# Kernel optimization log

Measured on AMD Instinct MI355X. Metric: run time of the kernel, lower is better.

Reference implementation:

```python
import jax, jax.numpy as jnp
import numpy as np

B, T, D = 32, 1024, 512
H = 1024          # hidden_size
LV = 128          # level_hidden_size
NREP = H // LV    # n_repeat = 8
NL = 2            # num_layers


def setup_inputs() -> dict:
    key = jax.random.key(0)
    ks = jax.random.split(key, 9)
    s = 0.02
    inp = {"x": jax.random.normal(ks[0], (B, T, D), jnp.float32)}
    # layer 0: input dim D; layer 1: input dim H
    inp["W_lstm0"] = jax.random.normal(ks[1], (4 * H, D + H), jnp.float32) * s
    inp["b_lstm0"] = jnp.zeros((4 * H,), jnp.float32)
    inp["W_lvl0"] = jax.random.normal(ks[2], (2 * LV, D + H), jnp.float32) * s
    inp["b_lvl0"] = jnp.zeros((2 * LV,), jnp.float32)
    inp["W_lstm1"] = jax.random.normal(ks[3], (4 * H, H + H), jnp.float32) * s
    inp["b_lstm1"] = jnp.zeros((4 * H,), jnp.float32)
    inp["W_lvl1"] = jax.random.normal(ks[4], (2 * LV, H + H), jnp.float32) * s
    inp["b_lvl1"] = jnp.zeros((2 * LV,), jnp.float32)
    return inp


def _cell(Wl, bl, Wv, bv, h, c, x_t):
    comb = jnp.concatenate([x_t, h], axis=-1)               # [B, in+H]
    gates = comb @ Wl.T + bl                                 # [B, 4H]
    cc_i, cc_f, cc_o, cc_g = jnp.split(gates, 4, axis=-1)
    lvl = comb @ Wv.T + bv                                   # [B, 2*LV]
    cc_i_h, cc_f_h = jnp.split(lvl, 2, axis=-1)
    i = jax.nn.sigmoid(cc_i)
    f = jax.nn.sigmoid(cc_f)
    o = jax.nn.sigmoid(cc_o)
    g = jnp.tanh(cc_g)
    p_f = jax.nn.softmax(cc_f_h, axis=-1)
    p_i = jax.nn.softmax(cc_i_h[..., ::-1], axis=-1)
    i_h = jnp.cumsum(p_f, axis=-1)                           # master input gate
    f_h = jnp.cumsum(p_i, axis=-1)[..., ::-1]                # master forget gate
    i_h = jnp.repeat(i_h, NREP, axis=-1)                     # [B, H]
    f_h = jnp.repeat(f_h, NREP, axis=-1)
    w = i_h * f_h
    c_new = w * (f * c + i * g) + (f_h - w) * c + (i_h - w) * g
    h_new = o * jnp.tanh(c_new)
    return h_new, c_new


def _run_layer(Wl, bl, Wv, bv, x):
    # x: [B, T, in]
    bsz = x.shape[0]
    h0 = jnp.zeros((bsz, H), x.dtype)
    c0 = jnp.zeros((bsz, H), x.dtype)

    def step(carry, x_t):
        h, c = carry
        h, c = _cell(Wl, bl, Wv, bv, h, c, x_t)
        return (h, c), h

    (_, _), hs = jax.lax.scan(step, (h0, c0), jnp.swapaxes(x, 0, 1))
    return jnp.swapaxes(hs, 0, 1)                            # [B, T, H]


def reference(x, W_lstm0, b_lstm0, W_lvl0, b_lvl0,
              W_lstm1, b_lstm1, W_lvl1, b_lvl1):
    out0 = _run_layer(W_lstm0, b_lstm0, W_lvl0, b_lvl0, x)
    out1 = _run_layer(W_lstm1, b_lstm1, W_lvl1, b_lvl1, out0)
    return out1
```

## Files before the change

kernel.cpp:

```cpp
#include <hip/hip_runtime.h>

namespace {
constexpr int kB  = 32;
constexpr int kT  = 1024;
constexpr int kD  = 512;
constexpr int kH  = 1024;
constexpr int kLV = 128;
constexpr int kNG = 4 * kH + 2 * kLV;
constexpr int kNBLK = 256;
constexpr int kNTHR = 512;
constexpr int kOffH0 = 8192;
constexpr int kOffWF = kOffH0 + 2 * kB * kH + 2 * kB * kNG;
constexpr int kRedOff = 3 * 1536 * 2 * 16;
constexpr int kIhOff  = kRedOff + 12288;
constexpr int kFhOff  = kIhOff + 512;
constexpr int kSmxOff = kFhOff + 512;
constexpr int kLdsBytes = kSmxOff + 32;
}

typedef float vfloat4 __attribute__((ext_vector_type(4)));
typedef float floatx4 __attribute__((ext_vector_type(4)));
typedef _Float16 half8_t __attribute__((ext_vector_type(8)));
typedef unsigned short ushort_t;

static __device__ __forceinline__ unsigned ld_flag(const unsigned* p) {
  return __hip_atomic_load(p, __ATOMIC_RELAXED, __HIP_MEMORY_SCOPE_AGENT);
}
static __device__ __forceinline__ void st_flag(unsigned* p, unsigned v) {
  __hip_atomic_store(p, v, __ATOMIC_RELAXED, __HIP_MEMORY_SCOPE_AGENT);
}
static __device__ __forceinline__ float ld_coh(const float* p) {
  return __hip_atomic_load(p, __ATOMIC_RELAXED, __HIP_MEMORY_SCOPE_AGENT);
}
static __device__ __forceinline__ void st_wt(float* p, float v) {
  asm volatile("global_store_dword %0, %1, off sc0 sc1" :: "v"(p), "v"(v) : "memory");
}
static __device__ __forceinline__ void st_wtu(unsigned* p, unsigned v) {
  asm volatile("global_store_dword %0, %1, off sc0 sc1" :: "v"(p), "v"(v) : "memory");
}
static __device__ __forceinline__ void ld8h(uint4 v[8], const ushort_t* b) {
  asm volatile(
      "global_load_dwordx4 %0, %8, off sc0 sc1\n\t"
      "global_load_dwordx4 %1, %8, off offset:256 sc0 sc1\n\t"
      "global_load_dwordx4 %2, %8, off offset:512 sc0 sc1\n\t"
      "global_load_dwordx4 %3, %8, off offset:768 sc0 sc1\n\t"
      "global_load_dwordx4 %4, %8, off offset:1024 sc0 sc1\n\t"
      "global_load_dwordx4 %5, %8, off offset:1280 sc0 sc1\n\t"
      "global_load_dwordx4 %6, %8, off offset:1536 sc0 sc1\n\t"
      "global_load_dwordx4 %7, %8, off offset:1792 sc0 sc1\n\t"
      "s_waitcnt vmcnt(0)"
      : "=&v"(v[0]), "=&v"(v[1]), "=&v"(v[2]), "=&v"(v[3]),
        "=&v"(v[4]), "=&v"(v[5]), "=&v"(v[6]), "=&v"(v[7])
      : "v"(b)
      : "memory");
}
static __device__ __forceinline__ void ld8h2(uint4 v[8], uint4 w[8],
                                             const ushort_t* b0, const ushort_t* b1) {
  asm volatile(
      "global_load_dwordx4 %0,  %16, off sc0 sc1\n\t"
      "global_load_dwordx4 %1,  %16, off offset:256 sc0 sc1\n\t"
      "global_load_dwordx4 %2,  %16, off offset:512 sc0 sc1\n\t"
      "global_load_dwordx4 %3,  %16, off offset:768 sc0 sc1\n\t"
      "global_load_dwordx4 %4,  %16, off offset:1024 sc0 sc1\n\t"
      "global_load_dwordx4 %5,  %16, off offset:1280 sc0 sc1\n\t"
      "global_load_dwordx4 %6,  %16, off offset:1536 sc0 sc1\n\t"
      "global_load_dwordx4 %7,  %16, off offset:1792 sc0 sc1\n\t"
      "global_load_dwordx4 %8,  %17, off sc0 sc1\n\t"
      "global_load_dwordx4 %9,  %17, off offset:256 sc0 sc1\n\t"
      "global_load_dwordx4 %10, %17, off offset:512 sc0 sc1\n\t"
      "global_load_dwordx4 %11, %17, off offset:768 sc0 sc1\n\t"
      "global_load_dwordx4 %12, %17, off offset:1024 sc0 sc1\n\t"
      "global_load_dwordx4 %13, %17, off offset:1280 sc0 sc1\n\t"
      "global_load_dwordx4 %14, %17, off offset:1536 sc0 sc1\n\t"
      "global_load_dwordx4 %15, %17, off offset:1792 sc0 sc1\n\t"
      "s_waitcnt vmcnt(0)"
      : "=&v"(v[0]), "=&v"(v[1]), "=&v"(v[2]), "=&v"(v[3]),
        "=&v"(v[4]), "=&v"(v[5]), "=&v"(v[6]), "=&v"(v[7]),
        "=&v"(w[0]), "=&v"(w[1]), "=&v"(w[2]), "=&v"(w[3]),
        "=&v"(w[4]), "=&v"(w[5]), "=&v"(w[6]), "=&v"(w[7])
      : "v"(b0), "v"(b1)
      : "memory");
}
static __device__ __forceinline__ unsigned pkrtz(float a, float b) {
  return __builtin_bit_cast(unsigned, __builtin_amdgcn_cvt_pkrtz(a, b));
}
static __device__ __forceinline__ uint4 pack2(vfloat4 a, vfloat4 b) {
  uint4 r;
  r.x = pkrtz(a.x, a.y); r.y = pkrtz(a.z, a.w);
  r.z = pkrtz(b.x, b.y); r.w = pkrtz(b.z, b.w);
  return r;
}
static __device__ __forceinline__ floatx4 mfma16(uint4 a, uint4 b, floatx4 c) {
  return __builtin_amdgcn_mfma_f32_16x16x32_f16(
      __builtin_bit_cast(half8_t, a), __builtin_bit_cast(half8_t, b), c, 0, 0, 0);
}

__global__ __launch_bounds__(256) void cvt_fp16_kernel(
    const float* __restrict__ src, ushort_t* __restrict__ dst, int n8) {
  int i = blockIdx.x * 256 + threadIdx.x;
  if (i >= n8) return;
  const vfloat4* s4 = (const vfloat4*)src;
  vfloat4 a = s4[2 * i], b = s4[2 * i + 1];
  typedef _Float16 h8 __attribute__((ext_vector_type(8)));
  h8 o;
  o[0] = (_Float16)a.x; o[1] = (_Float16)a.y;
  o[2] = (_Float16)a.z; o[3] = (_Float16)a.w;
  o[4] = (_Float16)b.x; o[5] = (_Float16)b.y;
  o[6] = (_Float16)b.z; o[7] = (_Float16)b.w;
  ((h8*)dst)[i] = o;
}

__global__ __launch_bounds__(kNTHR, 2) void onlstm_kernel(
    const float* __restrict__ x,
    const float* __restrict__ bl0, const float* __restrict__ bv0,
    const float* __restrict__ bl1, const float* __restrict__ bv1,
    const ushort_t* __restrict__ wf0u, const ushort_t* __restrict__ wf1u,
    float* __restrict__ out, float* __restrict__ ws)
{
  const int tid = threadIdx.x;
  const int bid = blockIdx.x;

  unsigned* flagA = (unsigned*)ws;
  unsigned* flagB = (unsigned*)ws + 4096;
  ushort_t* h0f = (ushort_t*)(ws + kOffH0);
  ushort_t* h1f = h0f + kB * kH;
  float* gates0 = ws + kOffH0 + kB * kH;
  float* gates1 = gates0 + kB * kNG;

  __shared__ __align__(16) char sb[kLdsBytes];
  uint4* wb4   = (uint4*)sb;
  float* redp  = (float*)(sb + kRedOff);
  float* ih_sh = (float*)(sb + kIhOff);
  float* fh_sh = (float*)(sb + kFhOff);
  float* smx   = (float*)(sb + kSmxOff);

  auto signal = [&](unsigned* arr, unsigned v) {
    asm volatile("s_waitcnt vmcnt(0)" ::: "memory");
    __syncthreads();
    if (tid == 0) st_flag(&arr[bid * 16], v);
  };
  auto wait_set = [&](unsigned* arr, int lo, int n, unsigned target) {
    if (tid < n) {
      while (ld_flag(&arr[(lo + tid) * 16]) != target)
        __builtin_amdgcn_s_sleep(2);
    }
    __syncthreads();
    asm volatile("" ::: "memory");
  };

  int L, ntile, cb0;
  if (bid < 32)       { L = 0; ntile = 3; cb0 = bid * 48; }
  else if (bid < 120) { L = 0; ntile = 2; cb0 = 1536 + (bid - 32) * 32; }
  else                { L = 1; ntile = 2; cb0 = (bid - 120) * 32; }
  const int K   = L ? 2048 : 1536;
  const int ts4 = K * 2;
  const bool three = (ntile == 3);
  const int rstride = three ? 3 : 2;
  const ushort_t* wf = L ? wf1u : wf0u;
  const float* blp = L ? bl1 : bl0;
  const float* bvp = L ? bv1 : bv0;
  float* gatesL = L ? gates1 : gates0;

  const int lane = tid & 63;
  const int rt   = (tid >> 6) & 1;
  const int str  = tid >> 7;
  const int r_   = rt * 16 + (lane & 15);
  const int koct = lane >> 4;
  const int colg0 = cb0 + (lane & 15);
  const int colg1 = cb0 + 16 + (lane & 15);
  const int colg2 = cb0 + 32 + (lane & 15);

  auto redsl = [&](int slot, int accIdx) -> float* {
    return &redp[(((slot * 2 + rt) * rstride) + accIdx) * 256 + lane * 4];
  };

  for (int tt = 0; tt < ntile; ++tt) {
    const int colb = cb0 + tt * 16;
    for (int idx = tid; idx < ts4; idx += kNTHR) {
      int m = idx >> 6, l2 = idx & 63;
      size_t off = (size_t)(colb + (l2 & 15)) * K + m * 32 + 8 * (l2 >> 4);
      wb4[tt * ts4 + idx] = *(const uint4*)(wf + off);
    }
  }
  const float b0w = (colg0 < 4096) ? blp[colg0] : bvp[colg0 - 4096];
  const float b1w = (colg1 < 4096) ? blp[colg1] : bvp[colg1 - 4096];
  const float b2w = three ? ((colg2 < 4096) ? blp[colg2] : bvp[colg2 - 4096]) : 0.f;
  __syncthreads();

  { int idx = bid * kNTHR + tid; if (idx < kB * kH) st_wtu((unsigned*)h0f + idx, 0u); }
  float creg = 0.f;
  signal(flagB, 1u);
  if (bid < 120) wait_set(flagB, 0, 128, 1u);
  else           wait_set(flagB, 0, 256, 1u);

  const int pbB  = (bid & 127) >> 2;
  const int qq4B = bid & 3;
  auto cellB = [&](const float* gbase, ushort_t* hb, float& cr, float* outp, int t) {
    const float* gr = gbase + (size_t)pbB * kNG;
    const int wl = tid & 63, wv2 = tid >> 6;
    const bool sm = tid < 128;
    const bool cl = tid < 256;
    float vi = 0.f, vf = 0.f, vo = 0.f, vg = 0.f;
    int j = qq4B * 256 + tid;
    if (cl) {
      vi = ld_coh(gr + j);
      vf = ld_coh(gr + kH + j);
      vo = ld_coh(gr + 2 * kH + j);
      vg = ld_coh(gr + 3 * kH + j);
    }
    float ai = 0.f, af = 0.f;
    if (sm) { ai = ld_coh(gr + 4096 + tid); af = ld_coh(gr + 4096 + kLV + tid); }
    float mi = ai, mf = af;
    if (sm) {
#pragma unroll
      for (int d2 = 32; d2 > 0; d2 >>= 1) {
        mi = fmaxf(mi, __shfl_xor(mi, d2));
        mf = fmaxf(mf, __shfl_xor(mf, d2));
      }
      if (wl == 0) { smx[wv2] = mi; smx[2 + wv2] = mf; }
    }
    __syncthreads();
    mi = fmaxf(smx[0], smx[1]);
    mf = fmaxf(smx[2], smx[3]);
    float ei = 0.f, Pi = 0.f, Pf = 0.f;
    if (sm) {
      ei = __expf(ai - mi);
      float ef = __expf(af - mf);
      Pi = ei; Pf = ef;
#pragma unroll
      for (int d2 = 1; d2 < 64; d2 <<= 1) {
        float ni = __shfl_up(Pi, d2);
        float nf = __shfl_up(Pf, d2);
        if (wl >= d2) { Pi += ni; Pf += nf; }
      }
      if (wl == 63) { smx[4 + wv2] = Pi; smx[6 + wv2] = Pf; }
    }
    __syncthreads();
    float Si = smx[4] + smx[5], Sf = smx[6] + smx[7];
    if (sm) {
      if (wv2 == 1) { Pi += smx[4]; Pf += smx[6]; }
      ih_sh[tid] = Pf / Sf;
      fh_sh[tid] = (Si - Pi + ei) / Si;
    }
    __syncthreads();
    if (cl) {
      float i_ = 1.f / (1.f + __expf(-vi));
      float f_ = 1.f / (1.f + __expf(-vf));
      float o_ = 1.f / (1.f + __expf(-vo));
      float g_ = tanhf(vg);
      int l2 = j >> 3;
      float ih = ih_sh[l2], fh = fh_sh[l2];
      float w  = ih * fh;
      float cold = cr;
      float cn = w * (f_ * cold + i_ * g_) + (fh - w) * cold + (ih - w) * g_;
      float hn = o_ * tanhf(cn);
      cr = cn;
      float hnn = __shfl_xor(hn, 1);
      if (!(tid & 1))
        st_wtu((unsigned*)hb + ((size_t)pbB * kH + j) / 2, pkrtz(hn, hnn));
      if (outp) st_wt(outp + ((size_t)pbB * kT + t) * kH + j, hn);
    }
  };

  for (int e = 0; e <= kT; ++e) {
    const bool actA = L ? (e >= 1) : (e < kT);

    if (actA) {
      floatx4 a0 = {0.f,0.f,0.f,0.f}, a1 = a0, a2 = a0;
      if (L == 0) {
        {
          const float* bx = x + ((size_t)r_ * kT + e) * kD + str * 32 + koct * 8;
          vfloat4 vx[8];
#pragma unroll
          for (int j = 0; j < 4; ++j) {
            vx[2*j]   = *(const vfloat4*)(bx + j * 128);
            vx[2*j+1] = *(const vfloat4*)(bx + j * 128 + 4);
          }
          uint4 pa[4];
#pragma unroll
          for (int j = 0; j < 4; ++j) pa[j] = pack2(vx[2*j], vx[2*j+1]);
#pragma unroll
          for (int j = 0; j < 4; ++j) {
            const int m = str + 4 * j;
            a0 = mfma16(pa[j], wb4[m * 64 + lane], a0);
            a1 = mfma16(pa[j], wb4[ts4 + m * 64 + lane], a1);
            if (three) a2 = mfma16(pa[j], wb4[2 * ts4 + m * 64 + lane], a2);
          }
        }
        {
          uint4 pa[8];
          ld8h(pa, h0f + (size_t)r_ * kH + str * 32 + koct * 8);
#pragma unroll
          for (int j = 0; j < 8; ++j) {
            const int m = 16 + str + 4 * j;
            a0 = mfma16(pa[j], wb4[m * 64 + lane], a0);
            a1 = mfma16(pa[j], wb4[ts4 + m * 64 + lane], a1);
            if (three) a2 = mfma16(pa[j], wb4[2 * ts4 + m * 64 + lane], a2);
          }
        }
      } else {
        uint4 pa[8], pb[8];
        ld8h2(pa, pb, h0f + (size_t)r_ * kH + str * 32 + koct * 8,
                      h1f + (size_t)r_ * kH + str * 32 + koct * 8);
#pragma unroll
        for (int j = 0; j < 8; ++j) {
          const int m = str + 4 * j;
          a0 = mfma16(pa[j], wb4[m * 64 + lane], a0);
          a1 = mfma16(pa[j], wb4[ts4 + m * 64 + lane], a1);
        }
#pragma unroll
        for (int j = 0; j < 8; ++j) {
          const int m = 32 + str + 4 * j;
          a0 = mfma16(pb[j], wb4[m * 64 + lane], a0);
          a1 = mfma16(pb[j], wb4[ts4 + m * 64 + lane], a1);
        }
      }
      if (!three) {
        if (str != 0) {
          *(floatx4*)redsl(str - 1, 0) = a0;
          *(floatx4*)redsl(str - 1, 1) = a1;
        }
        __syncthreads();
        if (str == 0) {
#pragma unroll
          for (int s2 = 0; s2 < 3; ++s2) {
            a0 += *(const floatx4*)redsl(s2, 0);
            a1 += *(const floatx4*)redsl(s2, 1);
          }
        }
      } else {
        if (str == 1 || str == 2) {
          *(floatx4*)redsl(str - 1, 0) = a0;
          *(floatx4*)redsl(str - 1, 1) = a1;
          *(floatx4*)redsl(str - 1, 2) = a2;
        }
        __syncthreads();
        if (str == 0) {
#pragma unroll
          for (int s2 = 0; s2 < 2; ++s2) {
            a0 += *(const floatx4*)redsl(s2, 0);
            a1 += *(const floatx4*)redsl(s2, 1);
            a2 += *(const floatx4*)redsl(s2, 2);
          }
        }
        __syncthreads();
        if (str == 3) {
          *(floatx4*)redsl(0, 0) = a0;
          *(floatx4*)redsl(0, 1) = a1;
          *(floatx4*)redsl(0, 2) = a2;
        }
        __syncthreads();
        if (str == 0) {
          a0 += *(const floatx4*)redsl(0, 0);
          a1 += *(const floatx4*)redsl(0, 1);
          a2 += *(const floatx4*)redsl(0, 2);
        }
      }
      if (str == 0) {
        const int rb = rt * 16 + koct * 4;
#pragma unroll
        for (int r = 0; r < 4; ++r)
          st_wt(gatesL + (size_t)(rb + r) * kNG + colg0, a0[r] + b0w);
#pragma unroll
        for (int r = 0; r < 4; ++r)
          st_wt(gatesL + (size_t)(rb + r) * kNG + colg1, a1[r] + b1w);
        if (three) {
#pragma unroll
          for (int r = 0; r < 4; ++r)
            st_wt(gatesL + (size_t)(rb + r) * kNG + colg2, a2[r] + b2w);
        }
      }
    }
    signal(flagA, (unsigned)(e + 1));
    if (bid < 128) wait_set(flagA, 0, 256, (unsigned)(e + 1));
    else           wait_set(flagA, 120, 136, (unsigned)(e + 1));

    if (bid < 128) {
      if (e < kT) cellB(gates0, h0f, creg, nullptr, e);
    } else {
      if (e >= 1) cellB(gates1, h1f, creg, out, e - 1);
    }
    signal(flagB, (unsigned)(e + 2));
    if (e < kT) {
      if (bid < 120) wait_set(flagB, 0, 128, (unsigned)(e + 2));
      else           wait_set(flagB, 0, 256, (unsigned)(e + 2));
    }
  }
}

extern "C" void kernel_launch(void* const* d_in, const int* in_sizes, int n_in,
                              void* d_out, int out_size, void* d_ws, size_t ws_size,
                              hipStream_t stream) {
  const float* x   = (const float*)d_in[0];
  const float* Wl0 = (const float*)d_in[1];
  const float* bl0 = (const float*)d_in[2];
  const float* Wv0 = (const float*)d_in[3];
  const float* bv0 = (const float*)d_in[4];
  const float* Wl1 = (const float*)d_in[5];
  const float* bl1 = (const float*)d_in[6];
  const float* Wv1 = (const float*)d_in[7];
  const float* bv1 = (const float*)d_in[8];
  (void)in_sizes; (void)n_in; (void)out_size; (void)ws_size;

  float* ws = (float*)d_ws;
  ushort_t* wf0 = (ushort_t*)(ws + kOffWF);
  ushort_t* wf1 = wf0 + (size_t)4352 * 1536;

  {
    int n;
    n = 4096 * 1536 / 8;
    cvt_fp16_kernel<<<(n + 255) / 256, 256, 0, stream>>>(Wl0, wf0, n);
    n = 256 * 1536 / 8;
    cvt_fp16_kernel<<<(n + 255) / 256, 256, 0, stream>>>(
        Wv0, wf0 + (size_t)4096 * 1536, n);
    n = 4096 * 2048 / 8;
    cvt_fp16_kernel<<<(n + 255) / 256, 256, 0, stream>>>(Wl1, wf1, n);
    n = 256 * 2048 / 8;
    cvt_fp16_kernel<<<(n + 255) / 256, 256, 0, stream>>>(
        Wv1, wf1 + (size_t)4096 * 2048, n);
  }

  onlstm_kernel<<<dim3(kNBLK), dim3(kNTHR), 0, stream>>>(
      x, bl0, bv0, bl1, bv1, wf0, wf1, (float*)d_out, ws);
}
```

Measured before the change: 10.88 ms.

## Double-buffer hidden state and relax grid barriers to overlap input projection

Double-buffers the fp16 hidden-state arrays by step parity so producers can write step e while consumers still read step e-1. The strict all-block equality waits become monotonic >= waits placed just before the h-dependent MFMAs, so the x-projection of layer 0 overlaps the wait. Layer-0 cell blocks now wait only on the flags they actually depend on. The level-gate softmax/cumsum is reduced to a single wavefront with two elements per lane, removing two block barriers. A sense-reversing init barrier resets flags so the kernel can be relaunched safely. Relaxed ordering increases the risk of subtle races.

```diff
diff --git a/kernel.cpp b/kernel.cpp
--- a/kernel.cpp
+++ b/kernel.cpp
@@ -9,13 +9,11 @@
 constexpr int kNG = 4 * kH + 2 * kLV;
 constexpr int kNBLK = 256;
 constexpr int kNTHR = 512;
-constexpr int kOffH0 = 8192;
-constexpr int kOffWF = kOffH0 + 2 * kB * kH + 2 * kB * kNG;
+constexpr int kOffH0 = 16384;
 constexpr int kRedOff = 3 * 1536 * 2 * 16;
 constexpr int kIhOff  = kRedOff + 12288;
 constexpr int kFhOff  = kIhOff + 512;
-constexpr int kSmxOff = kFhOff + 512;
-constexpr int kLdsBytes = kSmxOff + 32;
+constexpr int kLdsBytes = kFhOff + 512;
 }
 
 typedef float vfloat4 __attribute__((ext_vector_type(4)));
@@ -120,11 +118,13 @@
   const int tid = threadIdx.x;
   const int bid = blockIdx.x;
 
-  unsigned* flagA = (unsigned*)ws;
-  unsigned* flagB = (unsigned*)ws + 4096;
+  unsigned* flagA  = (unsigned*)ws;
+  unsigned* flagB  = (unsigned*)ws + 4096;
+  unsigned* cflags = (unsigned*)ws + 8192;
+  unsigned* cgenp  = (unsigned*)ws + 12288;
   ushort_t* h0f = (ushort_t*)(ws + kOffH0);
-  ushort_t* h1f = h0f + kB * kH;
-  float* gates0 = ws + kOffH0 + kB * kH;
+  ushort_t* h1f = h0f + 2 * kB * kH;
+  float* gates0 = (float*)(h1f + 2 * kB * kH);
   float* gates1 = gates0 + kB * kNG;
 
   __shared__ __align__(16) char sb[kLdsBytes];
@@ -132,19 +132,38 @@
   float* redp  = (float*)(sb + kRedOff);
   float* ih_sh = (float*)(sb + kIhOff);
   float* fh_sh = (float*)(sb + kFhOff);
-  float* smx   = (float*)(sb + kSmxOff);
 
   auto signal = [&](unsigned* arr, unsigned v) {
     asm volatile("s_waitcnt vmcnt(0)" ::: "memory");
     __syncthreads();
     if (tid == 0) st_flag(&arr[bid * 16], v);
   };
-  auto wait_set = [&](unsigned* arr, int lo, int n, unsigned target) {
+  auto wait_ge = [&](unsigned* arr, int lo, int n, int tgt) {
     if (tid < n) {
-      while (ld_flag(&arr[(lo + tid) * 16]) != target)
+      while ((int)(ld_flag(&arr[(lo + tid) * 16]) - (unsigned)tgt) < 0)
         __builtin_amdgcn_s_sleep(2);
     }
     __syncthreads();
+    asm volatile("" ::: "memory");
+  };
+  unsigned iseq = 0;
+  auto initbar = [&]() {
+    ++iseq;
+    asm volatile("s_waitcnt vmcnt(0)" ::: "memory");
+    __syncthreads();
+    if (bid == 0) {
+      if (tid >= 1 && tid < kNBLK) {
+        while (ld_flag(&cflags[tid * 16]) != iseq) __builtin_amdgcn_s_sleep(2);
+      }
+      __syncthreads();
+      if (tid == 0) st_flag(cgenp, iseq);
+    } else {
+      if (tid == 0) {
+        st_flag(&cflags[bid * 16], iseq);
+        while (ld_flag(cgenp) != iseq) __builtin_amdgcn_s_sleep(2);
+      }
+      __syncthreads();
+    }
     asm volatile("" ::: "memory");
   };
 
@@ -187,18 +206,17 @@
   const float b2w = three ? ((colg2 < 4096) ? blp[colg2] : bvp[colg2 - 4096]) : 0.f;
   __syncthreads();
 
-  { int idx = bid * kNTHR + tid; if (idx < kB * kH) st_wtu((unsigned*)h0f + idx, 0u); }
+  if (tid == 0) { st_flag(&flagA[bid * 16], 0u); st_flag(&flagB[bid * 16], 0u); }
+  { int idx = bid * kNTHR + tid;
+    if (idx < 65536) st_wtu((unsigned*)h0f + idx, 0u); }
   float creg = 0.f;
-  signal(flagB, 1u);
-  if (bid < 120) wait_set(flagB, 0, 128, 1u);
-  else           wait_set(flagB, 0, 256, 1u);
+  initbar();
+  initbar();
 
   const int pbB  = (bid & 127) >> 2;
   const int qq4B = bid & 3;
   auto cellB = [&](const float* gbase, ushort_t* hb, float& cr, float* outp, int t) {
     const float* gr = gbase + (size_t)pbB * kNG;
-    const int wl = tid & 63, wv2 = tid >> 6;
-    const bool sm = tid < 128;
     const bool cl = tid < 256;
     float vi = 0.f, vf = 0.f, vo = 0.f, vg = 0.f;
     int j = qq4B * 256 + tid;
@@ -208,39 +226,33 @@
       vo = ld_coh(gr + 2 * kH + j);
       vg = ld_coh(gr + 3 * kH + j);
     }
-    float ai = 0.f, af = 0.f;
-    if (sm) { ai = ld_coh(gr + 4096 + tid); af = ld_coh(gr + 4096 + kLV + tid); }
-    float mi = ai, mf = af;
-    if (sm) {
-#pragma unroll
-      for (int d2 = 32; d2 > 0; d2 >>= 1) {
-        mi = fmaxf(mi, __shfl_xor(mi, d2));
-        mf = fmaxf(mf, __shfl_xor(mf, d2));
-      }
-      if (wl == 0) { smx[wv2] = mi; smx[2 + wv2] = mf; }
-    }
-    __syncthreads();
-    mi = fmaxf(smx[0], smx[1]);
-    mf = fmaxf(smx[2], smx[3]);
-    float ei = 0.f, Pi = 0.f, Pf = 0.f;
-    if (sm) {
-      ei = __expf(ai - mi);
-      float ef = __expf(af - mf);
-      Pi = ei; Pf = ef;
-#pragma unroll
-      for (int d2 = 1; d2 < 64; d2 <<= 1) {
-        float ni = __shfl_up(Pi, d2);
-        float nf = __shfl_up(Pf, d2);
-        if (wl >= d2) { Pi += ni; Pf += nf; }
-      }
-      if (wl == 63) { smx[4 + wv2] = Pi; smx[6 + wv2] = Pf; }
-    }
-    __syncthreads();
-    float Si = smx[4] + smx[5], Sf = smx[6] + smx[7];
-    if (sm) {
-      if (wv2 == 1) { Pi += smx[4]; Pf += smx[6]; }
-      ih_sh[tid] = Pf / Sf;
-      fh_sh[tid] = (Si - Pi + ei) / Si;
+    if (tid < 64) {
+      float a0i = ld_coh(gr + 4096 + 2 * tid);
+      float a1i = ld_coh(gr + 4096 + 2 * tid + 1);
+      float a0f = ld_coh(gr + 4096 + kLV + 2 * tid);
+      float a1f = ld_coh(gr + 4096 + kLV + 2 * tid + 1);
+      float mi = fmaxf(a0i, a1i), mf = fmaxf(a0f, a1f);
+#pragma unroll
+      for (int d = 32; d > 0; d >>= 1) {
+        mi = fmaxf(mi, __shfl_xor(mi, d));
+        mf = fmaxf(mf, __shfl_xor(mf, d));
+      }
+      float e0i = __expf(a0i - mi), e1i = __expf(a1i - mi);
+      float e0f = __expf(a0f - mf), e1f = __expf(a1f - mf);
+      float si2 = e0i + e1i, sf2 = e0f + e1f;
+      float Pi = si2, Pf = sf2;
+#pragma unroll
+      for (int d = 1; d < 64; d <<= 1) {
+        float ni = __shfl_up(Pi, d);
+        float nf = __shfl_up(Pf, d);
+        if (tid >= d) { Pi += ni; Pf += nf; }
+      }
+      float Si = __shfl(Pi, 63), Sf = __shfl(Pf, 63);
+      float pri = Pi - si2, prf = Pf - sf2;
+      ih_sh[2 * tid]     = (prf + e0f) / Sf;
+      ih_sh[2 * tid + 1] = (prf + e0f + e1f) / Sf;
+      fh_sh[2 * tid]     = (Si - pri) / Si;
+      fh_sh[2 * tid + 1] = (Si - pri - e0i) / Si;
     }
     __syncthreads();
     if (cl) {
@@ -264,44 +276,48 @@
 
   for (int e = 0; e <= kT; ++e) {
     const bool actA = L ? (e >= 1) : (e < kT);
+    const size_t wpar = (size_t)(e & 1) * kB * kH;
+    const size_t rpar = (size_t)((e + 1) & 1) * kB * kH;
 
     if (actA) {
       floatx4 a0 = {0.f,0.f,0.f,0.f}, a1 = a0, a2 = a0;
       if (L == 0) {
-        {
-          const float* bx = x + ((size_t)r_ * kT + e) * kD + str * 32 + koct * 8;
-          vfloat4 vx[8];
-#pragma unroll
-          for (int j = 0; j < 4; ++j) {
-            vx[2*j]   = *(const vfloat4*)(bx + j * 128);
-            vx[2*j+1] = *(const vfloat4*)(bx + j * 128 + 4);
-          }
-          uint4 pa[4];
-#pragma unroll
-          for (int j = 0; j < 4; ++j) pa[j] = pack2(vx[2*j], vx[2*j+1]);
-#pragma unroll
-          for (int j = 0; j < 4; ++j) {
-            const int m = str + 4 * j;
-            a0 = mfma16(pa[j], wb4[m * 64 + lane], a0);
-            a1 = mfma16(pa[j], wb4[ts4 + m * 64 + lane], a1);
-            if (three) a2 = mfma16(pa[j], wb4[2 * ts4 + m * 64 + lane], a2);
-          }
-        }
-        {
-          uint4 pa[8];
-          ld8h(pa, h0f + (size_t)r_ * kH + str * 32 + koct * 8);
-#pragma unroll
-          for (int j = 0; j < 8; ++j) {
-            const int m = 16 + str + 4 * j;
-            a0 = mfma16(pa[j], wb4[m * 64 + lane], a0);
-            a1 = mfma16(pa[j], wb4[ts4 + m * 64 + lane], a1);
-            if (three) a2 = mfma16(pa[j], wb4[2 * ts4 + m * 64 + lane], a2);
-          }
+        const float* bx = x + ((size_t)r_ * kT + e) * kD + str * 32 + koct * 8;
+        vfloat4 vx[8];
+#pragma unroll
+        for (int j = 0; j < 4; ++j) {
+          vx[2*j]   = *(const vfloat4*)(bx + j * 128);
+          vx[2*j+1] = *(const vfloat4*)(bx + j * 128 + 4);
+        }
+        uint4 pa[4];
+#pragma unroll
+        for (int j = 0; j < 4; ++j) pa[j] = pack2(vx[2*j], vx[2*j+1]);
+#pragma unroll
+        for (int j = 0; j < 4; ++j) {
+          const int m = str + 4 * j;
+          a0 = mfma16(pa[j], wb4[m * 64 + lane], a0);
+          a1 = mfma16(pa[j], wb4[ts4 + m * 64 + lane], a1);
+          if (three) a2 = mfma16(pa[j], wb4[2 * ts4 + m * 64 + lane], a2);
+        }
+      }
+      if (e > 0) {
+        if (bid < 120) wait_ge(flagB, 0, 128, e + 1);
+        else           wait_ge(flagB, 0, 256, e + 1);
+      }
+      if (L == 0) {
+        uint4 pa[8];
+        ld8h(pa, h0f + rpar + (size_t)r_ * kH + str * 32 + koct * 8);
+#pragma unroll
+        for (int j = 0; j < 8; ++j) {
+          const int m = 16 + str + 4 * j;
+          a0 = mfma16(pa[j], wb4[m * 64 + lane], a0);
+          a1 = mfma16(pa[j], wb4[ts4 + m * 64 + lane], a1);
+          if (three) a2 = mfma16(pa[j], wb4[2 * ts4 + m * 64 + lane], a2);
         }
       } else {
         uint4 pa[8], pb[8];
-        ld8h2(pa, pb, h0f + (size_t)r_ * kH + str * 32 + koct * 8,
-                      h1f + (size_t)r_ * kH + str * 32 + koct * 8);
+        ld8h2(pa, pb, h0f + rpar + (size_t)r_ * kH + str * 32 + koct * 8,
+                      h1f + rpar + (size_t)r_ * kH + str * 32 + koct * 8);
 #pragma unroll
         for (int j = 0; j < 8; ++j) {
           const int m = str + 4 * j;
@@ -372,19 +388,25 @@
       }
     }
     signal(flagA, (unsigned)(e + 1));
-    if (bid < 128) wait_set(flagA, 0, 256, (unsigned)(e + 1));
-    else           wait_set(flagA, 120, 136, (unsigned)(e + 1));
 
     if (bid < 128) {
-      if (e < kT) cellB(gates0, h0f, creg, nullptr, e);
+      if (e < kT) {
+        if (tid < 256) {
+          int tgt = (tid < 120) ? e + 1 : e;
+          while ((int)(ld_flag(&flagA[tid * 16]) - (unsigned)tgt) < 0)
+            __builtin_amdgcn_s_sleep(2);
+        }
+        __syncthreads();
+        asm volatile("" ::: "memory");
+        cellB(gates0, h0f + wpar, creg, nullptr, e);
+      }
     } else {
-      if (e >= 1) cellB(gates1, h1f, creg, out, e - 1);
+      if (e >= 1) {
+        wait_ge(flagA, 120, 136, e + 1);
+        cellB(gates1, h1f + wpar, creg, out, e - 1);
+      }
     }
     signal(flagB, (unsigned)(e + 2));
-    if (e < kT) {
-      if (bid < 120) wait_set(flagB, 0, 128, (unsigned)(e + 2));
-      else           wait_set(flagB, 0, 256, (unsigned)(e + 2));
-    }
   }
 }
 
@@ -403,7 +425,10 @@
   (void)in_sizes; (void)n_in; (void)out_size; (void)ws_size;
 
   float* ws = (float*)d_ws;
-  ushort_t* wf0 = (ushort_t*)(ws + kOffWF);
+  float* gatesEnd = ws + kOffH0 + 65536 / 2 * 2;
+  (void)gatesEnd;
+  const size_t kOffWFf = (size_t)kOffH0 + 32768 + 32768 + 2 * (size_t)kB * kNG;
+  ushort_t* wf0 = (ushort_t*)(ws + kOffWFf);
   ushort_t* wf1 = wf0 + (size_t)4352 * 1536;
 
   {
```

After: 9.912 ms. 1.1x faster.
